# Kernel tuning notes

Hardware: AMD Instinct MI355X
Metric: run time of the kernel (lower is better)

The kernel has to match this reference:

```python
import jax, jax.numpy as jnp
from jax import lax
import numpy as np

B, C, H, W = 32, 128, 32, 32
ZDIM = 256
KH = KW = 3
NB_UNITS = C * C * KH * KW  # 147456
BN_EPS = 1e-6


def setup_inputs() -> dict:
    key = jax.random.key(0)
    ks = jax.random.split(key, 5)
    x = jax.random.normal(ks[0], (B, C, H, W), dtype=jnp.float32)
    z = jax.random.normal(ks[1], (B, ZDIM), dtype=jnp.float32)
    # glorot-uniform Dense kernel
    limit = np.sqrt(6.0 / (ZDIM + NB_UNITS)).astype(np.float32)
    dense_w = jax.random.uniform(ks[2], (ZDIM, NB_UNITS), dtype=jnp.float32,
                                 minval=-limit, maxval=limit)
    dense_b = jnp.zeros((NB_UNITS,), dtype=jnp.float32)
    # gamma initialized to +/- 0.02 (scale_for_weights)
    sign = jnp.where(jax.random.bernoulli(ks[3], 0.5, (NB_UNITS,)), 1.0, -1.0)
    gamma = (0.02 * sign).astype(jnp.float32)
    beta = jnp.zeros((NB_UNITS,), dtype=jnp.float32)
    b = jnp.zeros((C,), dtype=jnp.float32)  # deconv bias (zeros in original)
    return {"x": x, "z": z, "dense_w": dense_w, "dense_b": dense_b,
            "gamma": gamma, "beta": beta, "b": b}


def _per_sample_deconv(xi, wi):
    # xi: (C,H,W); wi: (C_in=stack, C_out=filter, KH, KW)
    # out[f,p,q] = sum_{s,u,v} xi[s, p+u-1, q+v-1] * wi[s,f,u,v]
    k = jnp.transpose(wi, (1, 0, 2, 3))  # OIHW: (f, s, u, v)
    y = lax.conv_general_dilated(xi[None], k, window_strides=(1, 1),
                                 padding=[(1, 1), (1, 1)],
                                 dimension_numbers=("NCHW", "OIHW", "NCHW"))
    return y[0]


def reference(x, z, dense_w, dense_b, gamma, beta, b):
    # hypernetwork: Dense(relu) -> BatchNorm(axis=1, batch stats) -> Reshape
    h = jax.nn.relu(z @ dense_w + dense_b)            # (B, NB_UNITS)
    mean = jnp.mean(h, axis=0)
    std = jnp.sqrt(jnp.var(h, axis=0))
    h = (h - mean) / (std + BN_EPS)
    h = gamma * h + beta
    Wk = h.reshape(B, C, C, KH, KW)                   # per-sample kernels (s,f,u,v)
    out = jax.vmap(_per_sample_deconv)(x, Wk)         # (B, C, H, W)
    out = out + b[None, :, None, None]
    return out + x                                    # residual add
```

## Files before the change

kernel.cpp:

```cpp
#include <hip/hip_runtime.h>

#define NB 147456
#define ZD 256
#define BSZ 32
#define CCH 128

typedef __attribute__((ext_vector_type(8))) short short8;
typedef __attribute__((ext_vector_type(16))) float floatx16;

__device__ __forceinline__ unsigned short f2bf(float f) {
    unsigned int u = __float_as_uint(f);
    return (unsigned short)((u + 0x7fffu + ((u >> 16) & 1u)) >> 16);
}
__device__ __forceinline__ unsigned pk(unsigned hi, unsigned lo) {
    return __builtin_amdgcn_perm(hi, lo, 0x07060302u);
}

__global__ __launch_bounds__(64) void hyper_mfma(
    const float* __restrict__ z, const float* __restrict__ dw,
    const float* __restrict__ db, const float* __restrict__ gamma,
    const float* __restrict__ beta, unsigned short* __restrict__ wkn)
{
    int lane = threadIdx.x;
    int L = lane & 31;
    int klane = lane >> 5;
    int n0 = blockIdx.x * 128 + 4 * L;

    short8 afrag[16];
    const float* zp = z + L * 256 + klane * 8;
#pragma unroll
    for (int s = 0; s < 16; s++) {
        float4 a0 = *(const float4*)(zp + s * 16);
        float4 a1 = *(const float4*)(zp + s * 16 + 4);
        uint4 u;
        u.x = pk(__float_as_uint(a0.y), __float_as_uint(a0.x));
        u.y = pk(__float_as_uint(a0.w), __float_as_uint(a0.z));
        u.z = pk(__float_as_uint(a1.y), __float_as_uint(a1.x));
        u.w = pk(__float_as_uint(a1.w), __float_as_uint(a1.z));
        afrag[s] = *(short8*)&u;
    }

    floatx16 acc[4];
#pragma unroll
    for (int t = 0; t < 4; t++)
#pragma unroll
        for (int r = 0; r < 16; r++) acc[t][r] = 0.f;

    const float* dwp = dw + (size_t)(klane * 8) * NB + n0;

    unsigned ba[8][4], bb[8][4];
#define LOADB(BUF, S)                                                         \
    _Pragma("unroll") for (int j = 0; j < 8; j++)                             \
        *(uint4*)&BUF[j][0] = *(const uint4*)(dwp + (size_t)((S) * 16 + j) * NB);
#define DOMFMA(BUF, S)                                                        \
    _Pragma("unroll") for (int t = 0; t < 4; t++) {                           \
        uint4 u;                                                              \
        u.x = pk(BUF[1][t], BUF[0][t]); u.y = pk(BUF[3][t], BUF[2][t]);       \
        u.z = pk(BUF[5][t], BUF[4][t]); u.w = pk(BUF[7][t], BUF[6][t]);       \
        acc[t] = __builtin_amdgcn_mfma_f32_32x32x16_bf16(                     \
            afrag[S], *(short8*)&u, acc[t], 0, 0, 0);                         \
    }
    LOADB(ba, 0)
#pragma unroll
    for (int s = 0; s < 16; s += 2) {
        LOADB(bb, s + 1)
        DOMFMA(ba, s)
        if (s + 2 < 16) LOADB(ba, s + 2)
        DOMFMA(bb, s + 1)
    }
#undef LOADB
#undef DOMFMA

    float4 bias = *(const float4*)(db + n0);
    float4 gmm  = *(const float4*)(gamma + n0);
    float4 btt  = *(const float4*)(beta + n0);
    float bias_a[4] = { bias.x, bias.y, bias.z, bias.w };
    float gm_a[4]   = { gmm.x, gmm.y, gmm.z, gmm.w };
    float bt_a[4]   = { btt.x, btt.y, btt.z, btt.w };

    float sc_a[4], mn_a[4];
#pragma unroll
    for (int t = 0; t < 4; t++) {
        float sp = 0.f, qp = 0.f;
#pragma unroll
        for (int r = 0; r < 16; r++) {
            float v = fmaxf(acc[t][r] + bias_a[t], 0.f);
            acc[t][r] = v;
            sp += v; qp += v * v;
        }
        sp += __shfl_xor(sp, 32, 64);
        qp += __shfl_xor(qp, 32, 64);
        float mn = sp * (1.f / 32.f);
        float var = fmaxf(qp * (1.f / 32.f) - mn * mn, 0.f);
        mn_a[t] = mn;
        sc_a[t] = gm_a[t] / (sqrtf(var) + 1e-6f);
    }

#pragma unroll
    for (int r = 0; r < 16; r++) {
        int brow = (r & 3) + 8 * (r >> 2) + 4 * klane;
        float w0 = sc_a[0] * (acc[0][r] - mn_a[0]) + bt_a[0];
        float w1 = sc_a[1] * (acc[1][r] - mn_a[1]) + bt_a[1];
        float w2 = sc_a[2] * (acc[2][r] - mn_a[2]) + bt_a[2];
        float w3 = sc_a[3] * (acc[3][r] - mn_a[3]) + bt_a[3];
        uint2 o;
        o.x = (unsigned)f2bf(w0) | ((unsigned)f2bf(w1) << 16);
        o.y = (unsigned)f2bf(w2) | ((unsigned)f2bf(w3) << 16);
        *(uint2*)&wkn[(size_t)brow * NB + n0] = o;
    }
}

__global__ __launch_bounds__(256) void repack_xt(
    const unsigned short* __restrict__ wkn, unsigned short* __restrict__ wkt,
    const float* __restrict__ x, unsigned short* __restrict__ xb16)
{
    __shared__ char lmem[16 * 580 * 4];
    int t = threadIdx.x;
    if (blockIdx.x < 256) {
        unsigned int* lt = (unsigned int*)lmem;
        int b = blockIdx.x >> 3;
        int s0 = (blockIdx.x & 7) * 16;
        const unsigned int* src = (const unsigned int*)wkn + ((size_t)b * NB >> 1) + (size_t)s0 * 576;
#pragma unroll
        for (int i = 0; i < 36; i++) {
            int idx = t + i * 256;
            int si = idx / 576;
            int j2 = idx - si * 576;
            lt[si * 580 + j2] = src[(size_t)si * 576 + j2];
        }
        __syncthreads();
        const unsigned short* ls = (const unsigned short*)lt;
#pragma unroll
        for (int i = 0; i < 9; i++) {
            int tau = t + i * 256;
            int half = tau & 1;
            int unit = tau >> 1;
            int uv = unit >> 7;
            int f = unit & 127;
            int col = f * 9 + uv;
            unsigned short v[8];
#pragma unroll
            for (int ss = 0; ss < 8; ss++)
                v[ss] = ls[(half * 8 + ss) * 1160 + col];
            uint4 o;
            o.x = v[0] | ((unsigned)v[1] << 16);
            o.y = v[2] | ((unsigned)v[3] << 16);
            o.z = v[4] | ((unsigned)v[5] << 16);
            o.w = v[6] | ((unsigned)v[7] << 16);
            ((uint4*)wkt)[((((size_t)b * 9 + uv) * 128 + f) * 16) + (s0 >> 3) + half] = o;
        }
    } else {
        unsigned short* lx = (unsigned short*)lmem;
        int idx = blockIdx.x - 256;
        int p = idx & 31;
        int b = idx >> 5;
        const float* xp = x + (size_t)b * CCH * 1024 + p * 32;
#pragma unroll
        for (int i = 0; i < 16; i++) {
            int ii = t + i * 256;
            int s = ii >> 5;
            int q = ii & 31;
            lx[q * 130 + s] = f2bf(xp[(size_t)s * 1024 + q]);
        }
        __syncthreads();
#pragma unroll
        for (int i = 0; i < 2; i++) {
            int tau = t + i * 256;
            int q = tau >> 4;
            int ch = tau & 15;
            const unsigned short* r = &lx[q * 130 + ch * 8];
            uint4 o;
            o.x = r[0] | ((unsigned)r[1] << 16);
            o.y = r[2] | ((unsigned)r[3] << 16);
            o.z = r[4] | ((unsigned)r[5] << 16);
            o.w = r[6] | ((unsigned)r[7] << 16);
            ((uint4*)xb16)[((((size_t)b * 32 + p) * 32) + q) * 16 + ch] = o;
        }
    }
}

__global__ __launch_bounds__(256) void conv_mfma(
    const float* __restrict__ x, const unsigned short* __restrict__ xb16,
    const unsigned short* __restrict__ wkt, const float* __restrict__ cb,
    float* __restrict__ out)
{
    __shared__ short8 lds8[6 * 34 * 17];
    int t = threadIdx.x;
    int w = blockIdx.x;
    int xcd = w & 7, slot = w >> 3;
    int b = (xcd << 2) | (slot & 3);
    int p0 = (slot >> 2) * 4;
    int wid = t >> 6, lane = t & 63;
    int fbase = (wid & 1) * 64;
    int rbase = (wid >> 1) * 2;
    int qcol = lane & 31, klane = lane >> 5;

    if (t < 192) {
        int r = t >> 5;
        int col = ((t >> 4) & 1) ? 33 : 0;
        int ch = t & 15;
        short8 zz = { 0, 0, 0, 0, 0, 0, 0, 0 };
        lds8[(r * 34 + col) * 17 + ch] = zz;
    }
    const uint4* xsrc = (const uint4*)xb16;
#pragma unroll
    for (int i = 0; i < 12; i++) {
        int tau = t + i * 256;
        int ch = tau & 15;
        int q = (tau >> 4) & 31;
        int r = tau >> 9;
        int prow = p0 - 1 + r;
        uint4 v = make_uint4(0, 0, 0, 0);
        if (prow >= 0 && prow < 32)
            v = xsrc[((((size_t)b * 32 + prow) * 32) + q) * 16 + ch];
        *(uint4*)&lds8[(r * 34 + q + 1) * 17 + ch] = v;
    }
    __syncthreads();

    floatx16 acc[2][2];
#pragma unroll
    for (int mi = 0; mi < 2; mi++)
#pragma unroll
        for (int ni = 0; ni < 2; ni++)
#pragma unroll
            for (int r = 0; r < 16; r++) acc[mi][ni][r] = 0.f;

    const short8* A8 = (const short8*)wkt + ((size_t)b * 9 << 11);
    short8 Abuf0[6], Abuf1[6];

#define LOAD6(BUF, ST)                                                        \
    {                                                                         \
        int v_ = (ST) >> 3, ks_ = (ST) & 7;                                   \
        int ko_ = ks_ * 2 + klane;                                            \
        _Pragma("unroll") for (int u_ = 0; u_ < 3; u_++) {                    \
            const short8* Au_ = A8 + ((size_t)(u_ * 3 + v_) << 11);           \
            BUF[u_ * 2]     = Au_[(fbase + qcol) * 16 + ko_];                 \
            BUF[u_ * 2 + 1] = Au_[(fbase + 32 + qcol) * 16 + ko_];            \
        }                                                                     \
    }
#define COMPUTE(BUF, ST)                                                      \
    {                                                                         \
        int v_ = (ST) >> 3, ks_ = (ST) & 7;                                   \
        int ko_ = ks_ * 2 + klane;                                            \
        short8 br[4];                                                         \
        _Pragma("unroll") for (int r_ = 0; r_ < 4; r_++)                      \
            br[r_] = lds8[((rbase + r_) * 34 + qcol + v_) * 17 + ko_];        \
        _Pragma("unroll") for (int u_ = 0; u_ < 3; u_++) {                    \
            acc[0][0] = __builtin_amdgcn_mfma_f32_32x32x16_bf16(              \
                BUF[u_ * 2], br[u_], acc[0][0], 0, 0, 0);                     \
            acc[0][1] = __builtin_amdgcn_mfma_f32_32x32x16_bf16(              \
                BUF[u_ * 2], br[u_ + 1], acc[0][1], 0, 0, 0);                 \
            acc[1][0] = __builtin_amdgcn_mfma_f32_32x32x16_bf16(              \
                BUF[u_ * 2 + 1], br[u_], acc[1][0], 0, 0, 0);                 \
            acc[1][1] = __builtin_amdgcn_mfma_f32_32x32x16_bf16(              \
                BUF[u_ * 2 + 1], br[u_ + 1], acc[1][1], 0, 0, 0);             \
        }                                                                     \
    }

    LOAD6(Abuf0, 0)
    for (int st = 0; st < 24; st += 2) {
        LOAD6(Abuf1, st + 1)
        COMPUTE(Abuf0, st)
        if (st + 2 < 24) LOAD6(Abuf0, st + 2)
        COMPUTE(Abuf1, st + 1)
    }
#undef LOAD6
#undef COMPUTE

    const size_t xb = (size_t)b * CCH * 1024;
    int prow0 = p0 + rbase;
#pragma unroll
    for (int mi = 0; mi < 2; mi++)
#pragma unroll
    for (int ni = 0; ni < 2; ni++) {
        int p = prow0 + ni;
#pragma unroll
        for (int r = 0; r < 16; r++) {
            int fl = (r & 3) + 8 * (r >> 2) + 4 * klane;
            int f = fbase + mi * 32 + fl;
            size_t idx = xb + (size_t)f * 1024 + p * 32 + qcol;
            out[idx] = acc[mi][ni][r] + x[idx] + cb[f];
        }
    }
}

extern "C" void kernel_launch(void* const* d_in, const int* in_sizes, int n_in,
                              void* d_out, int out_size, void* d_ws, size_t ws_size,
                              hipStream_t stream) {
    const float* x     = (const float*)d_in[0];
    const float* z     = (const float*)d_in[1];
    const float* dw    = (const float*)d_in[2];
    const float* db    = (const float*)d_in[3];
    const float* gamma = (const float*)d_in[4];
    const float* beta  = (const float*)d_in[5];
    const float* cb    = (const float*)d_in[6];
    float* out = (float*)d_out;

    unsigned short* wkn  = (unsigned short*)d_ws;
    unsigned short* wkt  = (unsigned short*)((char*)d_ws + (size_t)BSZ * NB * 2);
    unsigned short* xb16 = (unsigned short*)((char*)d_ws + (size_t)BSZ * NB * 4);

    hyper_mfma<<<NB / 128, 64, 0, stream>>>(z, dw, db, gamma, beta, wkn);
    repack_xt<<<256 + 1024, 256, 0, stream>>>(wkn, wkt, x, xb16);
    conv_mfma<<<256, 256, 0, stream>>>(x, xb16, wkt, cb, out);
}
```

Measured before the change: 290.6 us.

## Transpose weight/activation packing layouts and halve conv tile per block

Changes the repacked bf16 weight and activation layouts so that channel-chunk is the outer index and filter/column is innermost, making global loads coalesced across lanes. The conv kernel now processes 2 output rows per block with each wave owning 32 filters, doubling the grid to 512 blocks and halving accumulator and A-buffer registers. This aims for better occupancy and coalescing, at the cost of more redundant weight loads per output and a larger halo-to-work ratio.

New measurement: 270.5 us. -6.9%, faster.

```diff
diff --git a/kernel.cpp b/kernel.cpp
--- a/kernel.cpp
+++ b/kernel.cpp
@@ -133,10 +133,9 @@
 #pragma unroll
         for (int i = 0; i < 9; i++) {
             int tau = t + i * 256;
-            int half = tau & 1;
-            int unit = tau >> 1;
-            int uv = unit >> 7;
-            int f = unit & 127;
+            int f = tau & 127;
+            int half = (tau >> 7) & 1;
+            int uv = tau >> 8;
             int col = f * 9 + uv;
             unsigned short v[8];
 #pragma unroll
@@ -147,7 +146,7 @@
             o.y = v[2] | ((unsigned)v[3] << 16);
             o.z = v[4] | ((unsigned)v[5] << 16);
             o.w = v[6] | ((unsigned)v[7] << 16);
-            ((uint4*)wkt)[((((size_t)b * 9 + uv) * 128 + f) * 16) + (s0 >> 3) + half] = o;
+            ((uint4*)wkt)[((((size_t)b * 9 + uv) * 16) + (s0 >> 3) + half) * 128 + f] = o;
         }
     } else {
         unsigned short* lx = (unsigned short*)lmem;
@@ -166,15 +165,15 @@
 #pragma unroll
         for (int i = 0; i < 2; i++) {
             int tau = t + i * 256;
-            int q = tau >> 4;
-            int ch = tau & 15;
+            int q = tau & 31;
+            int ch = tau >> 5;
             const unsigned short* r = &lx[q * 130 + ch * 8];
             uint4 o;
             o.x = r[0] | ((unsigned)r[1] << 16);
             o.y = r[2] | ((unsigned)r[3] << 16);
             o.z = r[4] | ((unsigned)r[5] << 16);
             o.w = r[6] | ((unsigned)r[7] << 16);
-            ((uint4*)xb16)[((((size_t)b * 32 + p) * 32) + q) * 16 + ch] = o;
+            ((uint4*)xb16)[(((size_t)b * 32 + p) * 16 + ch) * 32 + q] = o;
         }
     }
 }
@@ -184,59 +183,53 @@
     const unsigned short* __restrict__ wkt, const float* __restrict__ cb,
     float* __restrict__ out)
 {
-    __shared__ short8 lds8[6 * 34 * 17];
+    __shared__ short8 lds8[4 * 16 * 34];
     int t = threadIdx.x;
     int w = blockIdx.x;
     int xcd = w & 7, slot = w >> 3;
     int b = (xcd << 2) | (slot & 3);
-    int p0 = (slot >> 2) * 4;
+    int p0 = (slot >> 2) * 2;
     int wid = t >> 6, lane = t & 63;
-    int fbase = (wid & 1) * 64;
-    int rbase = (wid >> 1) * 2;
+    int fbase = wid * 32;
     int qcol = lane & 31, klane = lane >> 5;
 
-    if (t < 192) {
+    if (t < 128) {
         int r = t >> 5;
-        int col = ((t >> 4) & 1) ? 33 : 0;
-        int ch = t & 15;
+        int ch = (t >> 1) & 15;
+        int col = (t & 1) * 33;
         short8 zz = { 0, 0, 0, 0, 0, 0, 0, 0 };
-        lds8[(r * 34 + col) * 17 + ch] = zz;
+        lds8[(r * 16 + ch) * 34 + col] = zz;
     }
     const uint4* xsrc = (const uint4*)xb16;
 #pragma unroll
-    for (int i = 0; i < 12; i++) {
+    for (int i = 0; i < 8; i++) {
         int tau = t + i * 256;
-        int ch = tau & 15;
-        int q = (tau >> 4) & 31;
+        int q = tau & 31;
+        int ch = (tau >> 5) & 15;
         int r = tau >> 9;
         int prow = p0 - 1 + r;
         uint4 v = make_uint4(0, 0, 0, 0);
         if (prow >= 0 && prow < 32)
-            v = xsrc[((((size_t)b * 32 + prow) * 32) + q) * 16 + ch];
-        *(uint4*)&lds8[(r * 34 + q + 1) * 17 + ch] = v;
+            v = xsrc[(((size_t)b * 32 + prow) * 16 + ch) * 32 + q];
+        *(uint4*)&lds8[(r * 16 + ch) * 34 + q + 1] = v;
     }
     __syncthreads();
 
-    floatx16 acc[2][2];
-#pragma unroll
-    for (int mi = 0; mi < 2; mi++)
-#pragma unroll
-        for (int ni = 0; ni < 2; ni++)
-#pragma unroll
-            for (int r = 0; r < 16; r++) acc[mi][ni][r] = 0.f;
+    floatx16 acc[2];
+#pragma unroll
+    for (int ni = 0; ni < 2; ni++)
+#pragma unroll
+        for (int r = 0; r < 16; r++) acc[ni][r] = 0.f;
 
     const short8* A8 = (const short8*)wkt + ((size_t)b * 9 << 11);
-    short8 Abuf0[6], Abuf1[6];
-
-#define LOAD6(BUF, ST)                                                        \
+    short8 Abuf0[3], Abuf1[3];
+
+#define LOAD3(BUF, ST)                                                        \
     {                                                                         \
         int v_ = (ST) >> 3, ks_ = (ST) & 7;                                   \
         int ko_ = ks_ * 2 + klane;                                            \
-        _Pragma("unroll") for (int u_ = 0; u_ < 3; u_++) {                    \
-            const short8* Au_ = A8 + ((size_t)(u_ * 3 + v_) << 11);           \
-            BUF[u_ * 2]     = Au_[(fbase + qcol) * 16 + ko_];                 \
-            BUF[u_ * 2 + 1] = Au_[(fbase + 32 + qcol) * 16 + ko_];            \
-        }                                                                     \
+        _Pragma("unroll") for (int u_ = 0; u_ < 3; u_++)                      \
+            BUF[u_] = A8[(((size_t)(u_ * 3 + v_) * 16 + ko_) << 7) + fbase + qcol]; \
     }
 #define COMPUTE(BUF, ST)                                                      \
     {                                                                         \
@@ -244,42 +237,35 @@
         int ko_ = ks_ * 2 + klane;                                            \
         short8 br[4];                                                         \
         _Pragma("unroll") for (int r_ = 0; r_ < 4; r_++)                      \
-            br[r_] = lds8[((rbase + r_) * 34 + qcol + v_) * 17 + ko_];        \
+            br[r_] = lds8[(r_ * 16 + ko_) * 34 + qcol + v_];                  \
         _Pragma("unroll") for (int u_ = 0; u_ < 3; u_++) {                    \
-            acc[0][0] = __builtin_amdgcn_mfma_f32_32x32x16_bf16(              \
-                BUF[u_ * 2], br[u_], acc[0][0], 0, 0, 0);                     \
-            acc[0][1] = __builtin_amdgcn_mfma_f32_32x32x16_bf16(              \
-                BUF[u_ * 2], br[u_ + 1], acc[0][1], 0, 0, 0);                 \
-            acc[1][0] = __builtin_amdgcn_mfma_f32_32x32x16_bf16(              \
-                BUF[u_ * 2 + 1], br[u_], acc[1][0], 0, 0, 0);                 \
-            acc[1][1] = __builtin_amdgcn_mfma_f32_32x32x16_bf16(              \
-                BUF[u_ * 2 + 1], br[u_ + 1], acc[1][1], 0, 0, 0);             \
+            acc[0] = __builtin_amdgcn_mfma_f32_32x32x16_bf16(                 \
+                BUF[u_], br[u_], acc[0], 0, 0, 0);                            \
+            acc[1] = __builtin_amdgcn_mfma_f32_32x32x16_bf16(                 \
+                BUF[u_], br[u_ + 1], acc[1], 0, 0, 0);                        \
         }                                                                     \
     }
 
-    LOAD6(Abuf0, 0)
+    LOAD3(Abuf0, 0)
     for (int st = 0; st < 24; st += 2) {
-        LOAD6(Abuf1, st + 1)
+        LOAD3(Abuf1, st + 1)
         COMPUTE(Abuf0, st)
-        if (st + 2 < 24) LOAD6(Abuf0, st + 2)
+        if (st + 2 < 24) LOAD3(Abuf0, st + 2)
         COMPUTE(Abuf1, st + 1)
     }
-#undef LOAD6
+#undef LOAD3
 #undef COMPUTE
 
     const size_t xb = (size_t)b * CCH * 1024;
-    int prow0 = p0 + rbase;
-#pragma unroll
-    for (int mi = 0; mi < 2; mi++)
 #pragma unroll
     for (int ni = 0; ni < 2; ni++) {
-        int p = prow0 + ni;
+        int p = p0 + ni;
 #pragma unroll
         for (int r = 0; r < 16; r++) {
             int fl = (r & 3) + 8 * (r >> 2) + 4 * klane;
-            int f = fbase + mi * 32 + fl;
+            int f = fbase + fl;
             size_t idx = xb + (size_t)f * 1024 + p * 32 + qcol;
-            out[idx] = acc[mi][ni][r] + x[idx] + cb[f];
+            out[idx] = acc[ni][r] + x[idx] + cb[f];
         }
     }
 }
@@ -302,5 +288,5 @@
 
     hyper_mfma<<<NB / 128, 64, 0, stream>>>(z, dw, db, gamma, beta, wkn);
     repack_xt<<<256 + 1024, 256, 0, stream>>>(wkn, wkt, x, xb16);
-    conv_mfma<<<256, 256, 0, stream>>>(x, xb16, wkt, cb, out);
-}
+    conv_mfma<<<512, 256, 0, stream>>>(x, xb16, wkt, cb, out);
+}
```
